# Optimization experiments

Hardware: AMD Instinct MI355X
Metric: run time of the kernel (lower is better)

## Reference

```python
import jax, jax.numpy as jnp
import numpy as np

B, D, U = 256, 2048, 2048  # batch, input_dim, units
EPS = 1e-8


def setup_inputs() -> dict:
    key = jax.random.key(0)
    ks = jax.random.split(key, 20)
    sd = 1.0 / np.sqrt(D)
    su = 1.0 / np.sqrt(U)
    inp = {
        'x': jax.random.normal(ks[0], (B, D), jnp.float32),
        'h_prev': jax.random.normal(ks[1], (B, U), jnp.float32),
        'c_prev': jax.random.normal(ks[2], (B, U), jnp.float32),
        'n_prev': jax.random.uniform(ks[3], (B, U), jnp.float32),
        'm_prev': jax.random.normal(ks[4], (B, U), jnp.float32),
        # input-to-gate weights (Dense with bias), keras layout [in, out]
        'Wz': jax.random.normal(ks[5], (D, U), jnp.float32) * sd,
        'Wi': jax.random.normal(ks[6], (D, U), jnp.float32) * sd,
        'Wf': jax.random.normal(ks[7], (D, U), jnp.float32) * sd,
        'Wo': jax.random.normal(ks[8], (D, U), jnp.float32) * sd,
        'bz': jnp.zeros((U,), jnp.float32),
        'bi': jnp.zeros((U,), jnp.float32),
        'bf': jnp.zeros((U,), jnp.float32),
        'bo': jnp.zeros((U,), jnp.float32),
        # recurrent weights (Dense without bias)
        'Uz': jax.random.normal(ks[9], (U, U), jnp.float32) * su,
        'Ui': jax.random.normal(ks[10], (U, U), jnp.float32) * su,
        'Uf': jax.random.normal(ks[11], (U, U), jnp.float32) * su,
        'Uo': jax.random.normal(ks[12], (U, U), jnp.float32) * su,
    }
    return inp


def reference(x, h_prev, c_prev, n_prev, m_prev,
              Wz, Wi, Wf, Wo, bz, bi, bf, bo, Uz, Ui, Uf, Uo):
    # fuse the 8 small GEMMs into 2 wide GEMMs (same math, gates split after)
    W = jnp.concatenate([Wz, Wi, Wf, Wo], axis=1)      # [D, 4U]
    Uc = jnp.concatenate([Uz, Ui, Uf, Uo], axis=1)     # [U, 4U]
    b = jnp.concatenate([bz, bi, bf, bo], axis=0)      # [4U]
    pre = x @ W + h_prev @ Uc + b                      # [B, 4U]
    z_tilde, i_tilde, f_tilde, o_tilde = jnp.split(pre, 4, axis=1)

    # exponential-gate stabilization (forget_gate_type='exponential')
    m_t = jnp.maximum(i_tilde + m_prev, i_tilde)
    i_t = jnp.exp(i_tilde - m_t)
    f_t = jnp.exp(f_tilde + m_prev - m_t)

    o_t = jax.nn.sigmoid(o_tilde)
    z_t = jnp.tanh(z_tilde)

    c_t = f_t * c_prev + i_t * z_t
    n_t = f_t * n_prev + i_t
    h_t = o_t * (c_t / (n_t + EPS))
    return jnp.stack([h_t, c_t, n_t, m_t], axis=0)  # [4, B, U]
```

## Files before the change

### kernel.cpp

```cpp
#include <hip/hip_runtime.h>
#include <cstdint>
#include <cstddef>

#define B_   256
#define D_   2048
#define U_   2048
#define NTOT 8192
#define BN   32
#define BK   64
#define KC   2048
#define ITERS (KC / BK)

typedef _Float16 half8 __attribute__((ext_vector_type(8)));
typedef float floatx16 __attribute__((ext_vector_type(16)));

__global__ __launch_bounds__(256) void prep_kernel(
    const float* __restrict__ x, const float* __restrict__ h,
    _Float16* __restrict__ Ahi)
{
    int gid   = blockIdx.x * 256 + threadIdx.x;
    int chunk = gid >> 8;
    int row   = gid & 255;
    int col0  = chunk * 8;
    const float* src = (col0 < D_) ? (x + row * D_ + col0)
                                   : (h + row * U_ + (col0 - D_));
    float4 v0 = *(const float4*)(src);
    float4 v1 = *(const float4*)(src + 4);
    float v[8] = {v0.x, v0.y, v0.z, v0.w, v1.x, v1.y, v1.z, v1.w};
    half8 hi;
#pragma unroll
    for (int i = 0; i < 8; ++i) hi[i] = (_Float16)v[i];
    *(half8*)(Ahi + (chunk * 256 + row) * 8) = hi;
}

__global__ __launch_bounds__(256, 2) void gemm_kernel(
    const _Float16* __restrict__ Ahi,
    const float* __restrict__ Wz, const float* __restrict__ Wi,
    const float* __restrict__ Wf, const float* __restrict__ Wo,
    const float* __restrict__ Uz, const float* __restrict__ Ui,
    const float* __restrict__ Uf, const float* __restrict__ Uo,
    float* __restrict__ P)
{
    const int t    = threadIdx.x;
    const int w    = t >> 6;
    const int lane = t & 63;
    const int lg   = lane >> 5;
    const int lm   = lane & 31;

    const int nblk = blockIdx.x;
    const int ks   = blockIdx.y;
    const int n0   = nblk * BN;
    const int g    = n0 >> 11;
    const int c0   = n0 & (U_ - 1);

    const float* wsel[8] = {Wz, Wi, Wf, Wo, Uz, Ui, Uf, Uo};
    const float* Bm = wsel[ks * 4 + g];
    const int chunk0 = ks * 256;

    const _Float16* a0p = Ahi +
        ((size_t)(chunk0 + lg) * 256 + (size_t)(w * 64 + lm)) * 8;

    const float* bp = Bm + (size_t)(lg * 8) * U_ + c0 + lm;

    floatx16 acc0 = {}, acc1 = {};

    half8 abuf0[2][4], abuf1[2][4];
    float bbuf[2][32];

#define LOAD_STEP(kk, buf)                                                    \
    {                                                                         \
        _Pragma("unroll")                                                     \
        for (int kin = 0; kin < 4; ++kin) {                                   \
            const _Float16* ap = a0p + ((size_t)(kk) * 8 + kin * 2) * 2048;   \
            abuf0[buf][kin] = *(const half8*)(ap);                            \
            abuf1[buf][kin] = *(const half8*)(ap + 256);                      \
        }                                                                     \
        _Pragma("unroll")                                                     \
        for (int kin = 0; kin < 4; ++kin)                                     \
            _Pragma("unroll")                                                 \
            for (int j = 0; j < 8; ++j)                                       \
                bbuf[buf][kin * 8 + j] =                                      \
                    bp[((size_t)(kk) * 64 + kin * 16 + j) * U_];              \
    }

    LOAD_STEP(0, 0);

#pragma unroll
    for (int kk = 0; kk < ITERS; ++kk) {
        const int cur = kk & 1;
        if (kk + 1 < ITERS) LOAD_STEP(kk + 1, cur ^ 1);

        half8 bf[4];
#pragma unroll
        for (int kin = 0; kin < 4; ++kin)
#pragma unroll
            for (int j = 0; j < 8; ++j)
                bf[kin][j] = (_Float16)bbuf[cur][kin * 8 + j];

#pragma unroll
        for (int kin = 0; kin < 4; ++kin) {
            acc0 = __builtin_amdgcn_mfma_f32_32x32x16_f16(abuf0[cur][kin], bf[kin], acc0, 0, 0, 0);
            acc1 = __builtin_amdgcn_mfma_f32_32x32x16_f16(abuf1[cur][kin], bf[kin], acc1, 0, 0, 0);
        }
    }
#undef LOAD_STEP

    float* Pks = P + (size_t)ks * ((size_t)B_ * NTOT);
#pragma unroll
    for (int r = 0; r < 16; ++r) {
        int m = w * 64 + 4 * lg + (r & 3) + 8 * (r >> 2);
        Pks[(size_t)m * NTOT + n0 + lm] = acc0[r];
    }
#pragma unroll
    for (int r = 0; r < 16; ++r) {
        int m = w * 64 + 32 + 4 * lg + (r & 3) + 8 * (r >> 2);
        Pks[(size_t)m * NTOT + n0 + lm] = acc1[r];
    }
}

__global__ __launch_bounds__(256) void gates_kernel(
    const float* __restrict__ P,
    const float* __restrict__ c_prev, const float* __restrict__ n_prev,
    const float* __restrict__ m_prev,
    const float* __restrict__ bz, const float* __restrict__ bi,
    const float* __restrict__ bf, const float* __restrict__ bo,
    float* __restrict__ out)
{
    const size_t PS = (size_t)B_ * NTOT;
    const int OS = B_ * U_;
    int gid = blockIdx.x * 256 + threadIdx.x;
    int m = gid >> 9;
    int u = (gid & 511) * 4;

    float pre[4][4];
#pragma unroll
    for (int gi = 0; gi < 4; ++gi) {
        const float* base = P + (size_t)m * NTOT + gi * U_ + u;
        float4 s0 = *(const float4*)(base);
        float4 s1 = *(const float4*)(base + PS);
        pre[gi][0] = s0.x + s1.x;
        pre[gi][1] = s0.y + s1.y;
        pre[gi][2] = s0.z + s1.z;
        pre[gi][3] = s0.w + s1.w;
    }
    float4 bzv = *(const float4*)(bz + u);
    float4 biv = *(const float4*)(bi + u);
    float4 bfv = *(const float4*)(bf + u);
    float4 bov = *(const float4*)(bo + u);
    float bza[4] = {bzv.x, bzv.y, bzv.z, bzv.w};
    float bia[4] = {biv.x, biv.y, biv.z, biv.w};
    float bfa[4] = {bfv.x, bfv.y, bfv.z, bfv.w};
    float boa[4] = {bov.x, bov.y, bov.z, bov.w};

    float4 cp4 = *(const float4*)(c_prev + m * U_ + u);
    float4 np4 = *(const float4*)(n_prev + m * U_ + u);
    float4 mp4 = *(const float4*)(m_prev + m * U_ + u);
    float cpa[4] = {cp4.x, cp4.y, cp4.z, cp4.w};
    float npa[4] = {np4.x, np4.y, np4.z, np4.w};
    float mpa[4] = {mp4.x, mp4.y, mp4.z, mp4.w};

    float hr[4], cr[4], nr[4], mr[4];
#pragma unroll
    for (int e = 0; e < 4; ++e) {
        float zt = pre[0][e] + bza[e];
        float it = pre[1][e] + bia[e];
        float ft = pre[2][e] + bfa[e];
        float ot = pre[3][e] + boa[e];
        float mp = mpa[e];
        float m_t = fmaxf(it + mp, it);
        float i_t = expf(it - m_t);
        float f_t = expf(ft + mp - m_t);
        float o_t = 1.0f / (1.0f + expf(-ot));
        float z_t = tanhf(zt);
        float c_t = f_t * cpa[e] + i_t * z_t;
        float n_t = f_t * npa[e] + i_t;
        float h_t = o_t * (c_t / (n_t + 1e-8f));
        hr[e] = h_t; cr[e] = c_t; nr[e] = n_t; mr[e] = m_t;
    }
    float4 hv = {hr[0], hr[1], hr[2], hr[3]};
    float4 cv = {cr[0], cr[1], cr[2], cr[3]};
    float4 nv = {nr[0], nr[1], nr[2], nr[3]};
    float4 mv = {mr[0], mr[1], mr[2], mr[3]};
    *(float4*)(out + 0 * OS + m * U_ + u) = hv;
    *(float4*)(out + 1 * OS + m * U_ + u) = cv;
    *(float4*)(out + 2 * OS + m * U_ + u) = nv;
    *(float4*)(out + 3 * OS + m * U_ + u) = mv;
}

extern "C" void kernel_launch(void* const* d_in, const int* in_sizes, int n_in,
                              void* d_out, int out_size, void* d_ws, size_t ws_size,
                              hipStream_t stream)
{
    const float* x  = (const float*)d_in[0];
    const float* h  = (const float*)d_in[1];
    const float* cp = (const float*)d_in[2];
    const float* np = (const float*)d_in[3];
    const float* mp = (const float*)d_in[4];
    const float* Wz = (const float*)d_in[5];
    const float* Wi = (const float*)d_in[6];
    const float* Wf = (const float*)d_in[7];
    const float* Wo = (const float*)d_in[8];
    const float* bz = (const float*)d_in[9];
    const float* bi = (const float*)d_in[10];
    const float* bf = (const float*)d_in[11];
    const float* bo = (const float*)d_in[12];
    const float* Uz = (const float*)d_in[13];
    const float* Ui = (const float*)d_in[14];
    const float* Uf = (const float*)d_in[15];
    const float* Uo = (const float*)d_in[16];

    float* P = (float*)d_ws;
    _Float16* Ahi = (_Float16*)((char*)d_ws + (size_t)2 * B_ * NTOT * sizeof(float));

    prep_kernel<<<512, 256, 0, stream>>>(x, h, Ahi);
    gemm_kernel<<<dim3(256, 2), 256, 0, stream>>>(Ahi,
        Wz, Wi, Wf, Wo, Uz, Ui, Uf, Uo, P);
    gates_kernel<<<512, 256, 0, stream>>>(P, cp, np, mp, bz, bi, bf, bo,
        (float*)d_out);
}
```

Baseline: 245.6 us.

## Stage GEMM tiles in LDS with async A loads and wider N tile

```diff
diff --git a/kernel.cpp b/kernel.cpp
--- a/kernel.cpp
+++ b/kernel.cpp
@@ -6,7 +6,7 @@
 #define D_   2048
 #define U_   2048
 #define NTOT 8192
-#define BN   32
+#define BN   64
 #define BK   64
 #define KC   2048
 #define ITERS (KC / BK)
@@ -33,7 +33,7 @@
     *(half8*)(Ahi + (chunk * 256 + row) * 8) = hi;
 }
 
-__global__ __launch_bounds__(256, 2) void gemm_kernel(
+__global__ __launch_bounds__(512, 2) void gemm_kernel(
     const _Float16* __restrict__ Ahi,
     const float* __restrict__ Wz, const float* __restrict__ Wi,
     const float* __restrict__ Wf, const float* __restrict__ Wo,
@@ -41,11 +41,16 @@
     const float* __restrict__ Uf, const float* __restrict__ Uo,
     float* __restrict__ P)
 {
+    __shared__ __align__(16) _Float16 sA[2][8 * 256 * 8];
+    __shared__ __align__(16) _Float16 sB[2][BK * BN];
+
     const int t    = threadIdx.x;
     const int w    = t >> 6;
     const int lane = t & 63;
     const int lg   = lane >> 5;
     const int lm   = lane & 31;
+    const int wm   = w >> 1;
+    const int wn   = w & 1;
 
     const int nblk = blockIdx.x;
     const int ks   = blockIdx.y;
@@ -57,64 +62,112 @@
     const float* Bm = wsel[ks * 4 + g];
     const int chunk0 = ks * 256;
 
-    const _Float16* a0p = Ahi +
-        ((size_t)(chunk0 + lg) * 256 + (size_t)(w * 64 + lm)) * 8;
-
-    const float* bp = Bm + (size_t)(lg * 8) * U_ + c0 + lm;
+    const _Float16* Ag = Ahi + (size_t)chunk0 * 2048
+                             + (size_t)(w * 4) * 512 + (size_t)lane * 8;
+
+    const float* Bg = Bm + (size_t)(w * 8) * U_ + c0 + lane;
+    const int swb = (lane * 128 + w * 16) ^ ((lane & 7) << 4);
+
+    const int aoff = lg * 4096 + (wm * 64 + lm) * 16;
 
     floatx16 acc0 = {}, acc1 = {};
-
-    half8 abuf0[2][4], abuf1[2][4];
-    float bbuf[2][32];
-
-#define LOAD_STEP(kk, buf)                                                    \
-    {                                                                         \
+    float rb0[8], rb1[8];
+
+#define ISSUE_A(tt, buf)                                                      \
+    {                                                                         \
+        _Pragma("unroll")                                                     \
+        for (int i = 0; i < 4; ++i)                                           \
+            __builtin_amdgcn_global_load_lds(                                 \
+                (const __attribute__((address_space(1))) void*)(              \
+                    Ag + (size_t)(tt) * 16384 + i * 512),                     \
+                (__attribute__((address_space(3))) void*)(                    \
+                    (char*)&sA[buf][0] + (w * 4 + i) * 1024 + lane * 16),     \
+                16, 0, 0);                                                    \
+    }
+
+#define ISSUE_B(tt, rb)                                                       \
+    {                                                                         \
+        _Pragma("unroll")                                                     \
+        for (int j = 0; j < 8; ++j)                                           \
+            rb[j] = Bg[((size_t)(tt) * 64 + j) * U_];                         \
+    }
+
+#define WRITE_B(rb, buf)                                                      \
+    {                                                                         \
+        half8 hv;                                                             \
+        _Pragma("unroll")                                                     \
+        for (int j = 0; j < 8; ++j) hv[j] = (_Float16)rb[j];                  \
+        *(half8*)((char*)&sB[buf][0] + swb) = hv;                             \
+    }
+
+#define COMPUTE(cur)                                                          \
+    {                                                                         \
+        const char* bA = (const char*)&sA[cur][0];                            \
+        const char* bB = (const char*)&sB[cur][0];                            \
+        half8 af0[4], af1[4], bfr[4];                                         \
         _Pragma("unroll")                                                     \
         for (int kin = 0; kin < 4; ++kin) {                                   \
-            const _Float16* ap = a0p + ((size_t)(kk) * 8 + kin * 2) * 2048;   \
-            abuf0[buf][kin] = *(const half8*)(ap);                            \
-            abuf1[buf][kin] = *(const half8*)(ap + 256);                      \
+            af0[kin] = *(const half8*)(bA + aoff + kin * 8192);               \
+            af1[kin] = *(const half8*)(bA + aoff + kin * 8192 + 512);         \
+            bfr[kin] = *(const half8*)(bB +                                   \
+                (((wn * 32 + lm) * 128 + kin * 32 + lg * 16)                  \
+                 ^ ((lm & 7) << 4)));                                         \
         }                                                                     \
-        _Pragma("unroll")                                                     \
-        for (int kin = 0; kin < 4; ++kin)                                     \
-            _Pragma("unroll")                                                 \
-            for (int j = 0; j < 8; ++j)                                       \
-                bbuf[buf][kin * 8 + j] =                                      \
-                    bp[((size_t)(kk) * 64 + kin * 16 + j) * U_];              \
-    }
-
-    LOAD_STEP(0, 0);
-
-#pragma unroll
-    for (int kk = 0; kk < ITERS; ++kk) {
-        const int cur = kk & 1;
-        if (kk + 1 < ITERS) LOAD_STEP(kk + 1, cur ^ 1);
-
-        half8 bf[4];
-#pragma unroll
-        for (int kin = 0; kin < 4; ++kin)
-#pragma unroll
-            for (int j = 0; j < 8; ++j)
-                bf[kin][j] = (_Float16)bbuf[cur][kin * 8 + j];
-
-#pragma unroll
-        for (int kin = 0; kin < 4; ++kin) {
-            acc0 = __builtin_amdgcn_mfma_f32_32x32x16_f16(abuf0[cur][kin], bf[kin], acc0, 0, 0, 0);
-            acc1 = __builtin_amdgcn_mfma_f32_32x32x16_f16(abuf1[cur][kin], bf[kin], acc1, 0, 0, 0);
-        }
-    }
-#undef LOAD_STEP
+        __builtin_amdgcn_s_setprio(1);                                        \
+        _Pragma("unroll")                                                     \
+        for (int kin = 0; kin < 4; ++kin) {                                   \
+            acc0 = __builtin_amdgcn_mfma_f32_32x32x16_f16(af0[kin], bfr[kin], acc0, 0, 0, 0); \
+            acc1 = __builtin_amdgcn_mfma_f32_32x32x16_f16(af1[kin], bfr[kin], acc1, 0, 0, 0); \
+        }                                                                     \
+        __builtin_amdgcn_s_setprio(0);                                        \
+    }
+
+    ISSUE_A(0, 0);
+    ISSUE_B(0, rb1);
+    ISSUE_B(1, rb0);
+    WRITE_B(rb1, 0);
+    asm volatile("s_waitcnt vmcnt(8) lgkmcnt(0)" ::: "memory");
+    __builtin_amdgcn_s_barrier();
+
+    for (int tt = 0; tt < ITERS - 2; tt += 2) {
+        ISSUE_A(tt + 1, 1);
+        ISSUE_B(tt + 2, rb1);
+        COMPUTE(0);
+        WRITE_B(rb0, 1);
+        asm volatile("s_waitcnt vmcnt(8) lgkmcnt(0)" ::: "memory");
+        __builtin_amdgcn_s_barrier();
+
+        ISSUE_A(tt + 2, 0);
+        ISSUE_B(tt + 3, rb0);
+        COMPUTE(1);
+        WRITE_B(rb1, 0);
+        asm volatile("s_waitcnt vmcnt(8) lgkmcnt(0)" ::: "memory");
+        __builtin_amdgcn_s_barrier();
+    }
+
+    ISSUE_A(ITERS - 1, 1);
+    COMPUTE(0);
+    WRITE_B(rb0, 1);
+    asm volatile("s_waitcnt vmcnt(0) lgkmcnt(0)" ::: "memory");
+    __builtin_amdgcn_s_barrier();
+    COMPUTE(1);
+
+#undef ISSUE_A
+#undef ISSUE_B
+#undef WRITE_B
+#undef COMPUTE
 
     float* Pks = P + (size_t)ks * ((size_t)B_ * NTOT);
+    const int ncol = n0 + wn * 32 + lm;
 #pragma unroll
     for (int r = 0; r < 16; ++r) {
-        int m = w * 64 + 4 * lg + (r & 3) + 8 * (r >> 2);
-        Pks[(size_t)m * NTOT + n0 + lm] = acc0[r];
+        int m = wm * 64 + 4 * lg + (r & 3) + 8 * (r >> 2);
+        Pks[(size_t)m * NTOT + ncol] = acc0[r];
     }
 #pragma unroll
     for (int r = 0; r < 16; ++r) {
-        int m = w * 64 + 32 + 4 * lg + (r & 3) + 8 * (r >> 2);
-        Pks[(size_t)m * NTOT + n0 + lm] = acc1[r];
+        int m = wm * 64 + 32 + 4 * lg + (r & 3) + 8 * (r >> 2);
+        Pks[(size_t)m * NTOT + ncol] = acc1[r];
     }
 }
 
@@ -213,7 +266,7 @@
     _Float16* Ahi = (_Float16*)((char*)d_ws + (size_t)2 * B_ * NTOT * sizeof(float));
 
     prep_kernel<<<512, 256, 0, stream>>>(x, h, Ahi);
-    gemm_kernel<<<dim3(256, 2), 256, 0, stream>>>(Ahi,
+    gemm_kernel<<<dim3(128, 2), 512, 0, stream>>>(Ahi,
         Wz, Wi, Wf, Wo, Uz, Ui, Uf, Uo, P);
     gates_kernel<<<512, 256, 0, stream>>>(P, cp, np, mp, bz, bi, bf, bo,
         (float*)d_out);
```

Result: faster. 205.9 us (-16.2%).

## Stage B tile through swizzled LDS shared by 8 waves, one MFMA tile per wave

Applied to the files above, without the earlier changes.

```diff
diff --git a/kernel.cpp b/kernel.cpp
--- a/kernel.cpp
+++ b/kernel.cpp
@@ -12,6 +12,7 @@
 #define ITERS (KC / BK)
 
 typedef _Float16 half8 __attribute__((ext_vector_type(8)));
+typedef _Float16 half4 __attribute__((ext_vector_type(4)));
 typedef float floatx16 __attribute__((ext_vector_type(16)));
 
 __global__ __launch_bounds__(256) void prep_kernel(
@@ -33,7 +34,7 @@
     *(half8*)(Ahi + (chunk * 256 + row) * 8) = hi;
 }
 
-__global__ __launch_bounds__(256, 2) void gemm_kernel(
+__global__ __launch_bounds__(512, 4) void gemm_kernel(
     const _Float16* __restrict__ Ahi,
     const float* __restrict__ Wz, const float* __restrict__ Wi,
     const float* __restrict__ Wf, const float* __restrict__ Wo,
@@ -41,6 +42,8 @@
     const float* __restrict__ Uf, const float* __restrict__ Uo,
     float* __restrict__ P)
 {
+    __shared__ __align__(16) _Float16 sB[2][BK * BN];
+
     const int t    = threadIdx.x;
     const int w    = t >> 6;
     const int lane = t & 63;
@@ -55,66 +58,99 @@
 
     const float* wsel[8] = {Wz, Wi, Wf, Wo, Uz, Ui, Uf, Uo};
     const float* Bm = wsel[ks * 4 + g];
-    const int chunk0 = ks * 256;
-
-    const _Float16* a0p = Ahi +
-        ((size_t)(chunk0 + lg) * 256 + (size_t)(w * 64 + lm)) * 8;
-
-    const float* bp = Bm + (size_t)(lg * 8) * U_ + c0 + lm;
-
-    floatx16 acc0 = {}, acc1 = {};
-
-    half8 abuf0[2][4], abuf1[2][4];
-    float bbuf[2][32];
-
-#define LOAD_STEP(kk, buf)                                                    \
-    {                                                                         \
-        _Pragma("unroll")                                                     \
-        for (int kin = 0; kin < 4; ++kin) {                                   \
-            const _Float16* ap = a0p + ((size_t)(kk) * 8 + kin * 2) * 2048;   \
-            abuf0[buf][kin] = *(const half8*)(ap);                            \
-            abuf1[buf][kin] = *(const half8*)(ap + 256);                      \
-        }                                                                     \
+
+    const _Float16* Ag = Ahi +
+        ((size_t)(ks * 256 + lg) * 256 + (size_t)(w * 32 + lm)) * 8;
+
+    const int scol = t & 31;
+    const int sk0  = (t >> 5) * 4;
+    const float* Bg = Bm + (size_t)sk0 * U_ + c0 + scol;
+    const int swb = scol * 128 + ((sk0 * 2) ^ ((scol & 7) << 4));
+    const int bswz = (lm & 7) << 4;
+
+    floatx16 acc = {};
+    half8 abA[4], abB[4];
+    float rbA[4], rbB[4];
+
+#define ISSUE_A(tt, ab)                                                       \
+    {                                                                         \
         _Pragma("unroll")                                                     \
         for (int kin = 0; kin < 4; ++kin)                                     \
-            _Pragma("unroll")                                                 \
-            for (int j = 0; j < 8; ++j)                                       \
-                bbuf[buf][kin * 8 + j] =                                      \
-                    bp[((size_t)(kk) * 64 + kin * 16 + j) * U_];              \
-    }
-
-    LOAD_STEP(0, 0);
-
-#pragma unroll
-    for (int kk = 0; kk < ITERS; ++kk) {
-        const int cur = kk & 1;
-        if (kk + 1 < ITERS) LOAD_STEP(kk + 1, cur ^ 1);
-
-        half8 bf[4];
-#pragma unroll
-        for (int kin = 0; kin < 4; ++kin)
-#pragma unroll
-            for (int j = 0; j < 8; ++j)
-                bf[kin][j] = (_Float16)bbuf[cur][kin * 8 + j];
-
-#pragma unroll
-        for (int kin = 0; kin < 4; ++kin) {
-            acc0 = __builtin_amdgcn_mfma_f32_32x32x16_f16(abuf0[cur][kin], bf[kin], acc0, 0, 0, 0);
-            acc1 = __builtin_amdgcn_mfma_f32_32x32x16_f16(abuf1[cur][kin], bf[kin], acc1, 0, 0, 0);
-        }
-    }
-#undef LOAD_STEP
+            ab[kin] = *(const half8*)(Ag +                                    \
+                ((size_t)(tt) * 8 + kin * 2) * 2048);                         \
+    }
+
+#define ISSUE_B(tt, rb)                                                       \
+    {                                                                         \
+        _Pragma("unroll")                                                     \
+        for (int j = 0; j < 4; ++j)                                           \
+            rb[j] = Bg[((size_t)(tt) * 64 + j) * U_];                         \
+    }
+
+#define WRITE_B(rb, buf)                                                      \
+    {                                                                         \
+        half4 hv;                                                             \
+        _Pragma("unroll")                                                     \
+        for (int j = 0; j < 4; ++j) hv[j] = (_Float16)rb[j];                  \
+        *(half4*)((char*)&sB[buf][0] + swb) = hv;                             \
+    }
+
+#define COMPUTE(ab, buf)                                                      \
+    {                                                                         \
+        const char* bB = (const char*)&sB[buf][0];                            \
+        half8 bfr[4];                                                         \
+        _Pragma("unroll")                                                     \
+        for (int kin = 0; kin < 4; ++kin)                                     \
+            bfr[kin] = *(const half8*)(bB + lm * 128 +                        \
+                ((kin * 32 + lg * 16) ^ bswz));                               \
+        __builtin_amdgcn_s_setprio(1);                                        \
+        _Pragma("unroll")                                                     \
+        for (int kin = 0; kin < 4; ++kin)                                     \
+            acc = __builtin_amdgcn_mfma_f32_32x32x16_f16(ab[kin], bfr[kin],   \
+                                                         acc, 0, 0, 0);       \
+        __builtin_amdgcn_s_setprio(0);                                        \
+    }
+
+    ISSUE_B(0, rbA);
+    ISSUE_A(0, abA);
+    ISSUE_B(1, rbB);
+    WRITE_B(rbA, 0);
+    asm volatile("s_waitcnt vmcnt(4) lgkmcnt(0)" ::: "memory");
+    __builtin_amdgcn_s_barrier();
+
+    for (int tt = 0; tt < ITERS - 2; tt += 2) {
+        ISSUE_A(tt + 1, abB);
+        ISSUE_B(tt + 2, rbA);
+        COMPUTE(abA, 0);
+        WRITE_B(rbB, 1);
+        asm volatile("s_waitcnt vmcnt(4) lgkmcnt(0)" ::: "memory");
+        __builtin_amdgcn_s_barrier();
+
+        ISSUE_A(tt + 2, abA);
+        ISSUE_B(tt + 3, rbB);
+        COMPUTE(abB, 1);
+        WRITE_B(rbA, 0);
+        asm volatile("s_waitcnt vmcnt(4) lgkmcnt(0)" ::: "memory");
+        __builtin_amdgcn_s_barrier();
+    }
+
+    ISSUE_A(ITERS - 1, abB);
+    COMPUTE(abA, 0);
+    WRITE_B(rbB, 1);
+    asm volatile("s_waitcnt vmcnt(0) lgkmcnt(0)" ::: "memory");
+    __builtin_amdgcn_s_barrier();
+    COMPUTE(abB, 1);
+
+#undef ISSUE_A
+#undef ISSUE_B
+#undef WRITE_B
+#undef COMPUTE
 
     float* Pks = P + (size_t)ks * ((size_t)B_ * NTOT);
 #pragma unroll
     for (int r = 0; r < 16; ++r) {
-        int m = w * 64 + 4 * lg + (r & 3) + 8 * (r >> 2);
-        Pks[(size_t)m * NTOT + n0 + lm] = acc0[r];
-    }
-#pragma unroll
-    for (int r = 0; r < 16; ++r) {
-        int m = w * 64 + 32 + 4 * lg + (r & 3) + 8 * (r >> 2);
-        Pks[(size_t)m * NTOT + n0 + lm] = acc1[r];
+        int m = w * 32 + 4 * lg + (r & 3) + 8 * (r >> 2);
+        Pks[(size_t)m * NTOT + n0 + lm] = acc[r];
     }
 }
 
@@ -213,7 +249,7 @@
     _Float16* Ahi = (_Float16*)((char*)d_ws + (size_t)2 * B_ * NTOT * sizeof(float));
 
     prep_kernel<<<512, 256, 0, stream>>>(x, h, Ahi);
-    gemm_kernel<<<dim3(256, 2), 256, 0, stream>>>(Ahi,
+    gemm_kernel<<<dim3(256, 2), 512, 0, stream>>>(Ahi,
         Wz, Wi, Wf, Wo, Uz, Ui, Uf, Uo, P);
     gates_kernel<<<512, 256, 0, stream>>>(P, cp, np, mp, bz, bi, bf, bo,
         (float*)d_out);
```

After: 227.4 us. -7.4%, faster.
